# Kernel tuning notes

Measured on AMD Instinct MI355X. Metric: run time of the kernel, lower is better.

Reference implementation:

```python
import jax, jax.numpy as jnp
import numpy as np

N = 50000      # num nodes
E = 800000     # num edges (before self loops)
H = 2          # heads
C = 64         # out_channels (== in_dim, extra_layer=False)
L = 3          # n_layer
SLOPE = 0.2    # leaky_relu negative_slope


def setup_inputs() -> dict:
    key = jax.random.key(0)
    k1, k2, k3 = jax.random.split(key, 3)
    x = jax.random.normal(k1, (N, C), dtype=jnp.float32)
    edge_index = jax.random.randint(k2, (2, E), 0, N)
    att = jax.random.normal(k3, (L, H, C), dtype=jnp.float32) * 0.1  # glorot-ish scale
    bias = jnp.zeros((L, C), dtype=jnp.float32)
    return {"x": x, "edge_index": edge_index, "att": att, "bias": bias}


def _segment_softmax(alpha, dst, n):
    # alpha: [Etot, H], softmax over edges sharing the same destination node
    m = jax.ops.segment_max(alpha, dst, num_segments=n)          # [N, H]
    a = jnp.exp(alpha - m[dst])                                  # [Etot, H]
    s = jax.ops.segment_sum(a, dst, num_segments=n)              # [N, H]
    return a / (s[dst] + 1e-16)


def _gat_layer(x, src, dst, att_l, bias_l):
    # extra_layer=False: x_l == x_r == x broadcast over heads, so x_i + x_j is
    # head-independent; compute it once as [Etot, C].
    m = jax.nn.leaky_relu(x[dst] + x[src], negative_slope=SLOPE)  # [Etot, C]
    alpha = m @ att_l.T                                           # [Etot, H]
    alpha = _segment_softmax(alpha, dst, N)
    # message = x_j * alpha, scatter-add to destinations, then mean over heads
    outs = [jax.ops.segment_sum(x[src] * alpha[:, h:h + 1], dst, num_segments=N)
            for h in range(H)]                                    # H x [N, C]
    return jnp.stack(outs, 0).mean(0) + bias_l                    # [N, C]


def reference(x, edge_index, att, bias):
    # add self loops (add_self_loops=True)
    loops = jnp.arange(N, dtype=edge_index.dtype)
    src = jnp.concatenate([edge_index[0], loops])
    dst = jnp.concatenate([edge_index[1], loops])
    feats = [x]
    h = x
    for l in range(L):
        h = _gat_layer(h, src, dst, att[l], bias[l])
        feats.append(h)
    return jnp.stack(feats, axis=1).mean(axis=1)  # [N, C]
```

## Files before the change

### kernel.cpp

```cpp
#include <hip/hip_runtime.h>
#include <hip/hip_bf16.h>

#define NN 50000
#define EE 800000
#define CC 64
#define HH 2
#define LL 3
#define CAP 64
#define NB 782
#define BCAP 1280
#define CHUNK 8192
#define NBLK ((EE + CHUNK - 1) / CHUNK)



__global__ __launch_bounds__(1024) void k_bin(const int* __restrict__ ei,
                                              int* __restrict__ bcnt,
                                              unsigned int* __restrict__ bucket) {
    __shared__ unsigned int stash[CHUNK];
    __shared__ int hist[NB];
    __shared__ int rank[NB];
    __shared__ int base[NB];

    int c0 = blockIdx.x * CHUNK;
    int n = EE - c0; if (n > CHUNK) n = CHUNK;

    for (int b = threadIdx.x; b < NB; b += 1024) { hist[b] = 0; rank[b] = 0; }
    __syncthreads();

    for (int k = threadIdx.x; k < n; k += 1024) {
        unsigned int s = (unsigned int)ei[c0 + k];
        unsigned int d = (unsigned int)ei[EE + c0 + k];
        stash[k] = (d << 16) | s;
        atomicAdd(&hist[d >> 6], 1);
    }
    __syncthreads();

    for (int b = threadIdx.x; b < NB; b += 1024) {
        int c = hist[b];
        base[b] = c ? atomicAdd(&bcnt[b], c) : 0;
    }
    __syncthreads();

    for (int k = threadIdx.x; k < n; k += 1024) {
        unsigned int pk = stash[k];
        int b = (int)(pk >> 22);
        int r = atomicAdd(&rank[b], 1);
        int pos = base[b] + r;
        if (pos < BCAP) bucket[(size_t)b * BCAP + pos] = pk;
    }
}

__global__ __launch_bounds__(256) void k_place(const unsigned int* __restrict__ bucket,
                                               const int* __restrict__ bcnt,
                                               int* __restrict__ cnt,
                                               unsigned short* __restrict__ slots) {
    __shared__ int lcnt[64];
    int b = blockIdx.x;
    if (threadIdx.x < 64) lcnt[threadIdx.x] = 0;
    __syncthreads();
    int node0 = b << 6;
    int m = bcnt[b];
    if (m > BCAP) m = BCAP;
    const unsigned int* src = bucket + (size_t)b * BCAP;
    for (int i = threadIdx.x; i < m; i += 256) {
        unsigned int pk = src[i];
        int d = (int)(pk >> 16);
        int s = (int)(pk & 0xFFFFu);
        int pos = atomicAdd(&lcnt[d - node0], 1);
        if (pos < CAP) slots[(size_t)d * CAP + pos] = (unsigned short)s;
    }
    __syncthreads();
    if (threadIdx.x < 64) {
        int node = node0 + threadIdx.x;
        if (node < NN) cnt[node] = lcnt[threadIdx.x];
    }
}


typedef float v2f __attribute__((ext_vector_type(2)));

template <int CTRL>
__device__ __forceinline__ float dpp_add(float v) {
    int t = __builtin_amdgcn_update_dpp(0, __float_as_int(v), CTRL, 0xF, 0xF, true);
    return v + __int_as_float(t);
}

__device__ __forceinline__ float red16(float v) {
    v = dpp_add<0xB1>(v);
    v = dpp_add<0x4E>(v);
    v = dpp_add<0x141>(v);
    v = dpp_add<0x140>(v);
    return v;
}

__device__ __forceinline__ v2f lk2(v2f v) {
    v2f t = 0.2f * v;
    return __builtin_elementwise_max(v, t);
}

__device__ __forceinline__ v2f fma2(v2f a, v2f b, v2f c) {
    return __builtin_elementwise_fma(a, b, c);
}

template <bool FIRST>
__global__ __launch_bounds__(256) void k_gat(const float* __restrict__ h,
                                             const int* __restrict__ cnt,
                                             const unsigned short* __restrict__ slots,
                                             const float* __restrict__ att_l,
                                             const float* __restrict__ bias_l,
                                             float* __restrict__ h_out,
                                             float* __restrict__ acc, int n) {
    int wid = threadIdx.x >> 6;
    int lane = threadIdx.x & 63;
    int node = blockIdx.x * 4 + wid;
    if (node >= n) return;
    int sub = lane >> 4, q = lane & 15;
    unsigned qb = (unsigned)q << 4;
    const char* hb = (const char*)h;
    const v2f* attv = (const v2f*)att_l;
    v2f a0_01 = attv[2 * q],      a0_23 = attv[2 * q + 1];
    v2f a1_01 = attv[32 + 2 * q], a1_23 = attv[32 + 2 * q + 1];
    float4 hd = *(const float4*)(hb + (((unsigned)node << 8) + qb));
    v2f hd01 = {hd.x, hd.y}, hd23 = {hd.z, hd.w};
    int deg = cnt[node];
    if (deg > CAP) deg = CAP;
    const unsigned* rowu = (const unsigned*)(slots + (size_t)node * CAP);

    float s0, s1;
    v2f A0_01, A0_23, A1_01, A1_23;

    {
        v2f u01 = lk2(hd01 + hd01), u23 = lk2(hd23 + hd23);
        v2f d0 = fma2(u23, a0_23, u01 * a0_01);
        v2f d1 = fma2(u23, a1_23, u01 * a1_01);
        float p0 = red16(d0.x + d0.y);
        float p1 = red16(d1.x + d1.y);
        float e0 = 0.25f * __expf(p0), e1 = 0.25f * __expf(p1);
        s0 = e0; s1 = e1;
        A0_01 = e0 * hd01; A0_23 = e0 * hd23;
        A1_01 = e1 * hd01; A1_23 = e1 * hd23;
    }

    int npair = deg >> 1;
#pragma unroll 2
    for (int p = sub; p < npair; p += 4) {
        unsigned pk = rowu[p];
        float4 va = *(const float4*)(hb + (((pk & 0xFFFFu) << 8) + qb));
        float4 vb = *(const float4*)(hb + (((pk >> 16) << 8) + qb));
        v2f va01 = {va.x, va.y}, va23 = {va.z, va.w};
        v2f vb01 = {vb.x, vb.y}, vb23 = {vb.z, vb.w};
        v2f ma01 = lk2(va01 + hd01), ma23 = lk2(va23 + hd23);
        v2f mb01 = lk2(vb01 + hd01), mb23 = lk2(vb23 + hd23);
        v2f da0 = fma2(ma23, a0_23, ma01 * a0_01);
        v2f da1 = fma2(ma23, a1_23, ma01 * a1_01);
        v2f db0 = fma2(mb23, a0_23, mb01 * a0_01);
        v2f db1 = fma2(mb23, a1_23, mb01 * a1_01);
        float pa0 = red16(da0.x + da0.y);
        float pa1 = red16(da1.x + da1.y);
        float pb0 = red16(db0.x + db0.y);
        float pb1 = red16(db1.x + db1.y);
        float ea0 = __expf(pa0), ea1 = __expf(pa1);
        float eb0 = __expf(pb0), eb1 = __expf(pb1);
        s0 += ea0 + eb0;
        s1 += ea1 + eb1;
        v2f ea0v = {ea0, ea0}, ea1v = {ea1, ea1};
        v2f eb0v = {eb0, eb0}, eb1v = {eb1, eb1};
        A0_01 = fma2(ea0v, va01, fma2(eb0v, vb01, A0_01));
        A0_23 = fma2(ea0v, va23, fma2(eb0v, vb23, A0_23));
        A1_01 = fma2(ea1v, va01, fma2(eb1v, vb01, A1_01));
        A1_23 = fma2(ea1v, va23, fma2(eb1v, vb23, A1_23));
    }

    if (deg & 1) {
        int t = deg - 1;
        if (sub == ((t >> 1) & 3)) {
            unsigned s = ((const unsigned short*)rowu)[t];
            float4 hv = *(const float4*)(hb + ((s << 8) + qb));
            v2f hv01 = {hv.x, hv.y}, hv23 = {hv.z, hv.w};
            v2f m01 = lk2(hv01 + hd01), m23 = lk2(hv23 + hd23);
            v2f d0 = fma2(m23, a0_23, m01 * a0_01);
            v2f d1 = fma2(m23, a1_23, m01 * a1_01);
            float p0 = red16(d0.x + d0.y);
            float p1 = red16(d1.x + d1.y);
            float e0 = __expf(p0), e1 = __expf(p1);
            s0 += e0; s1 += e1;
            v2f e0v = {e0, e0}, e1v = {e1, e1};
            A0_01 = fma2(e0v, hv01, A0_01); A0_23 = fma2(e0v, hv23, A0_23);
            A1_01 = fma2(e1v, hv01, A1_01); A1_23 = fma2(e1v, hv23, A1_23);
        }
    }

#pragma unroll
    for (int step = 16; step <= 32; step <<= 1) {
        s0 += __shfl_xor(s0, step);
        s1 += __shfl_xor(s1, step);
        A0_01.x += __shfl_xor(A0_01.x, step); A0_01.y += __shfl_xor(A0_01.y, step);
        A0_23.x += __shfl_xor(A0_23.x, step); A0_23.y += __shfl_xor(A0_23.y, step);
        A1_01.x += __shfl_xor(A1_01.x, step); A1_01.y += __shfl_xor(A1_01.y, step);
        A1_23.x += __shfl_xor(A1_23.x, step); A1_23.y += __shfl_xor(A1_23.y, step);
    }

    if (sub == 0) {
        float inv0 = 0.5f / (s0 + 1e-16f);
        float inv1 = 0.5f / (s1 + 1e-16f);
        float4 b4 = ((const float4*)bias_l)[q];
        float4 o;
        o.x = A0_01.x * inv0 + A1_01.x * inv1 + b4.x;
        o.y = A0_01.y * inv0 + A1_01.y * inv1 + b4.y;
        o.z = A0_23.x * inv0 + A1_23.x * inv1 + b4.z;
        o.w = A0_23.y * inv0 + A1_23.y * inv1 + b4.w;
        ((float4*)h_out)[(size_t)node * 16 + q] = o;
        float4* accp = (float4*)acc + (size_t)node * 16 + q;
        float4 ac;
        if (FIRST) {
            ac.x = 0.25f * (hd.x + o.x); ac.y = 0.25f * (hd.y + o.y);
            ac.z = 0.25f * (hd.z + o.z); ac.w = 0.25f * (hd.w + o.w);
        } else {
            ac = *accp;
            ac.x += 0.25f * o.x; ac.y += 0.25f * o.y;
            ac.z += 0.25f * o.z; ac.w += 0.25f * o.w;
        }
        *accp = ac;
    }
}


static inline size_t align256(size_t x) { return (x + 255) & ~(size_t)255; }

extern "C" void kernel_launch(void* const* d_in, const int* in_sizes, int n_in,
                              void* d_out, int out_size, void* d_ws, size_t ws_size,
                              hipStream_t stream) {
    const float* x    = (const float*)d_in[0];
    const int*   ei   = (const int*)d_in[1];
    const float* att  = (const float*)d_in[2];
    const float* bias = (const float*)d_in[3];
    float* acc = (float*)d_out;

    char* w = (char*)d_ws;
    int* bcnt   = (int*)w;              w += align256((size_t)NB * sizeof(int));
    int* cnt    = (int*)w;              w += align256((size_t)NN * sizeof(int));
    unsigned int* bucket = (unsigned int*)w;
    w += align256((size_t)NB * BCAP * sizeof(unsigned int));
    unsigned short* slots = (unsigned short*)w;
    w += align256((size_t)NN * CAP * sizeof(unsigned short));
    float* hA   = (float*)w;            w += align256((size_t)NN * CC * sizeof(float));
    float* hB   = (float*)w;            w += align256((size_t)NN * CC * sizeof(float));

    const int B = 256;

    hipMemsetAsync(bcnt, 0, (size_t)NB * sizeof(int), stream);
    k_bin<<<NBLK, 1024, 0, stream>>>(ei, bcnt, bucket);
    k_place<<<NB, B, 0, stream>>>(bucket, bcnt, cnt, slots);

    k_gat<true><<<(NN + 3) / 4, B, 0, stream>>>(
        x, cnt, slots, att, bias, hA, acc, NN);
    k_gat<false><<<(NN + 3) / 4, B, 0, stream>>>(
        hA, cnt, slots, att + (size_t)HH * CC, bias + CC, hB, acc, NN);
    k_gat<false><<<(NN + 3) / 4, B, 0, stream>>>(
        hB, cnt, slots, att + (size_t)2 * HH * CC, bias + 2 * CC, hA, acc, NN);
}
```

Before: 196.1 us.

## Store node features in fp16 to halve gather traffic in GAT layers

Converts the input features to fp16 in a new kernel and keeps all intermediate layer outputs in fp16, so each gathered neighbor row is 128 bytes instead of 256. The lane mapping changes from 16 lanes x 4 floats to 8 lanes x 8 halves, giving 8 edge-pairs in flight per wave, with a new cross-group reduction. The last layer no longer writes its unused hidden output. This reduces memory bandwidth on the random gathers but adds fp16 rounding error that compounds across layers, plus an extra conversion launch.

```diff
diff --git a/kernel.cpp b/kernel.cpp
--- a/kernel.cpp
+++ b/kernel.cpp
@@ -1,5 +1,5 @@
 #include <hip/hip_runtime.h>
-#include <hip/hip_bf16.h>
+#include <hip/hip_fp16.h>
 
 #define NN 50000
 #define EE 800000
@@ -77,6 +77,17 @@
     }
 }
 
+__global__ __launch_bounds__(256) void k_cvt(const float* __restrict__ x,
+                                             unsigned short* __restrict__ x16) {
+    int i = blockIdx.x * 256 + threadIdx.x;
+    if (i >= NN * CC / 4) return;
+    float4 v = ((const float4*)x)[i];
+    __half2 h0 = __float22half2_rn((float2){v.x, v.y});
+    __half2 h1 = __float22half2_rn((float2){v.z, v.w});
+    uint2 u = {__builtin_bit_cast(unsigned, h0), __builtin_bit_cast(unsigned, h1)};
+    ((uint2*)x16)[i] = u;
+}
+
 
 typedef float v2f __attribute__((ext_vector_type(2)));
 
@@ -86,11 +97,17 @@
     return v + __int_as_float(t);
 }
 
-__device__ __forceinline__ float red16(float v) {
+__device__ __forceinline__ float red8(float v) {
     v = dpp_add<0xB1>(v);
     v = dpp_add<0x4E>(v);
     v = dpp_add<0x141>(v);
-    v = dpp_add<0x140>(v);
+    return v;
+}
+
+__device__ __forceinline__ float merge8(float v) {
+    v = dpp_add<0x128>(v);
+    v += __shfl_xor(v, 16);
+    v += __shfl_xor(v, 32);
     return v;
 }
 
@@ -103,125 +120,175 @@
     return __builtin_elementwise_fma(a, b, c);
 }
 
-template <bool FIRST>
-__global__ __launch_bounds__(256) void k_gat(const float* __restrict__ h,
+__device__ __forceinline__ void ldrow(const char* hbq, unsigned idx, v2f v[4]) {
+    uint4 u = *(const uint4*)(hbq + ((size_t)idx << 7));
+    float2 f0 = __half22float2(__builtin_bit_cast(__half2, u.x));
+    float2 f1 = __half22float2(__builtin_bit_cast(__half2, u.y));
+    float2 f2 = __half22float2(__builtin_bit_cast(__half2, u.z));
+    float2 f3 = __half22float2(__builtin_bit_cast(__half2, u.w));
+    v[0] = (v2f){f0.x, f0.y}; v[1] = (v2f){f1.x, f1.y};
+    v[2] = (v2f){f2.x, f2.y}; v[3] = (v2f){f3.x, f3.y};
+}
+
+template <bool FIRST, bool WRITE>
+__global__ __launch_bounds__(256) void k_gat(const unsigned short* __restrict__ hin,
+                                             const float* __restrict__ xf,
                                              const int* __restrict__ cnt,
                                              const unsigned short* __restrict__ slots,
                                              const float* __restrict__ att_l,
                                              const float* __restrict__ bias_l,
-                                             float* __restrict__ h_out,
+                                             unsigned short* __restrict__ hout,
                                              float* __restrict__ acc, int n) {
     int wid = threadIdx.x >> 6;
     int lane = threadIdx.x & 63;
     int node = blockIdx.x * 4 + wid;
     if (node >= n) return;
-    int sub = lane >> 4, q = lane & 15;
-    unsigned qb = (unsigned)q << 4;
-    const char* hb = (const char*)h;
+    int sub = lane >> 3;
+    unsigned t = (unsigned)(lane & 7);
+    const char* hbq = (const char*)hin + (t << 4);
     const v2f* attv = (const v2f*)att_l;
-    v2f a0_01 = attv[2 * q],      a0_23 = attv[2 * q + 1];
-    v2f a1_01 = attv[32 + 2 * q], a1_23 = attv[32 + 2 * q + 1];
-    float4 hd = *(const float4*)(hb + (((unsigned)node << 8) + qb));
-    v2f hd01 = {hd.x, hd.y}, hd23 = {hd.z, hd.w};
+    v2f a0[4], a1[4];
+#pragma unroll
+    for (int k = 0; k < 4; ++k) {
+        a0[k] = attv[4 * t + k];
+        a1[k] = attv[32 + 4 * t + k];
+    }
+    v2f hd[4];
+    ldrow(hbq, (unsigned)node, hd);
     int deg = cnt[node];
     if (deg > CAP) deg = CAP;
     const unsigned* rowu = (const unsigned*)(slots + (size_t)node * CAP);
 
     float s0, s1;
-    v2f A0_01, A0_23, A1_01, A1_23;
+    v2f A0[4], A1[4];
 
     {
-        v2f u01 = lk2(hd01 + hd01), u23 = lk2(hd23 + hd23);
-        v2f d0 = fma2(u23, a0_23, u01 * a0_01);
-        v2f d1 = fma2(u23, a1_23, u01 * a1_01);
-        float p0 = red16(d0.x + d0.y);
-        float p1 = red16(d1.x + d1.y);
-        float e0 = 0.25f * __expf(p0), e1 = 0.25f * __expf(p1);
+        v2f u[4];
+#pragma unroll
+        for (int k = 0; k < 4; ++k) u[k] = lk2(hd[k] + hd[k]);
+        v2f d0 = u[0] * a0[0], d1 = u[0] * a1[0];
+#pragma unroll
+        for (int k = 1; k < 4; ++k) {
+            d0 = fma2(u[k], a0[k], d0);
+            d1 = fma2(u[k], a1[k], d1);
+        }
+        float p0 = red8(d0.x + d0.y);
+        float p1 = red8(d1.x + d1.y);
+        float e0 = 0.125f * __expf(p0), e1 = 0.125f * __expf(p1);
         s0 = e0; s1 = e1;
-        A0_01 = e0 * hd01; A0_23 = e0 * hd23;
-        A1_01 = e1 * hd01; A1_23 = e1 * hd23;
+#pragma unroll
+        for (int k = 0; k < 4; ++k) { A0[k] = e0 * hd[k]; A1[k] = e1 * hd[k]; }
     }
 
     int npair = deg >> 1;
-#pragma unroll 2
-    for (int p = sub; p < npair; p += 4) {
+#pragma unroll 1
+    for (int p = sub; p < npair; p += 8) {
         unsigned pk = rowu[p];
-        float4 va = *(const float4*)(hb + (((pk & 0xFFFFu) << 8) + qb));
-        float4 vb = *(const float4*)(hb + (((pk >> 16) << 8) + qb));
-        v2f va01 = {va.x, va.y}, va23 = {va.z, va.w};
-        v2f vb01 = {vb.x, vb.y}, vb23 = {vb.z, vb.w};
-        v2f ma01 = lk2(va01 + hd01), ma23 = lk2(va23 + hd23);
-        v2f mb01 = lk2(vb01 + hd01), mb23 = lk2(vb23 + hd23);
-        v2f da0 = fma2(ma23, a0_23, ma01 * a0_01);
-        v2f da1 = fma2(ma23, a1_23, ma01 * a1_01);
-        v2f db0 = fma2(mb23, a0_23, mb01 * a0_01);
-        v2f db1 = fma2(mb23, a1_23, mb01 * a1_01);
-        float pa0 = red16(da0.x + da0.y);
-        float pa1 = red16(da1.x + da1.y);
-        float pb0 = red16(db0.x + db0.y);
-        float pb1 = red16(db1.x + db1.y);
+        v2f va[4], vb[4];
+        ldrow(hbq, pk & 0xFFFFu, va);
+        ldrow(hbq, pk >> 16, vb);
+        v2f ma[4], mb[4];
+#pragma unroll
+        for (int k = 0; k < 4; ++k) {
+            ma[k] = lk2(va[k] + hd[k]);
+            mb[k] = lk2(vb[k] + hd[k]);
+        }
+        v2f da0 = ma[0] * a0[0], da1 = ma[0] * a1[0];
+        v2f db0 = mb[0] * a0[0], db1 = mb[0] * a1[0];
+#pragma unroll
+        for (int k = 1; k < 4; ++k) {
+            da0 = fma2(ma[k], a0[k], da0); da1 = fma2(ma[k], a1[k], da1);
+            db0 = fma2(mb[k], a0[k], db0); db1 = fma2(mb[k], a1[k], db1);
+        }
+        float pa0 = red8(da0.x + da0.y);
+        float pa1 = red8(da1.x + da1.y);
+        float pb0 = red8(db0.x + db0.y);
+        float pb1 = red8(db1.x + db1.y);
         float ea0 = __expf(pa0), ea1 = __expf(pa1);
         float eb0 = __expf(pb0), eb1 = __expf(pb1);
         s0 += ea0 + eb0;
         s1 += ea1 + eb1;
         v2f ea0v = {ea0, ea0}, ea1v = {ea1, ea1};
         v2f eb0v = {eb0, eb0}, eb1v = {eb1, eb1};
-        A0_01 = fma2(ea0v, va01, fma2(eb0v, vb01, A0_01));
-        A0_23 = fma2(ea0v, va23, fma2(eb0v, vb23, A0_23));
-        A1_01 = fma2(ea1v, va01, fma2(eb1v, vb01, A1_01));
-        A1_23 = fma2(ea1v, va23, fma2(eb1v, vb23, A1_23));
+#pragma unroll
+        for (int k = 0; k < 4; ++k) {
+            A0[k] = fma2(ea0v, va[k], fma2(eb0v, vb[k], A0[k]));
+            A1[k] = fma2(ea1v, va[k], fma2(eb1v, vb[k], A1[k]));
+        }
     }
 
     if (deg & 1) {
-        int t = deg - 1;
-        if (sub == ((t >> 1) & 3)) {
-            unsigned s = ((const unsigned short*)rowu)[t];
-            float4 hv = *(const float4*)(hb + ((s << 8) + qb));
-            v2f hv01 = {hv.x, hv.y}, hv23 = {hv.z, hv.w};
-            v2f m01 = lk2(hv01 + hd01), m23 = lk2(hv23 + hd23);
-            v2f d0 = fma2(m23, a0_23, m01 * a0_01);
-            v2f d1 = fma2(m23, a1_23, m01 * a1_01);
-            float p0 = red16(d0.x + d0.y);
-            float p1 = red16(d1.x + d1.y);
+        int te = deg - 1;
+        if (sub == ((te >> 1) & 7)) {
+            unsigned s = ((const unsigned short*)rowu)[te];
+            v2f hv[4];
+            ldrow(hbq, s, hv);
+            v2f m[4];
+#pragma unroll
+            for (int k = 0; k < 4; ++k) m[k] = lk2(hv[k] + hd[k]);
+            v2f d0 = m[0] * a0[0], d1 = m[0] * a1[0];
+#pragma unroll
+            for (int k = 1; k < 4; ++k) {
+                d0 = fma2(m[k], a0[k], d0);
+                d1 = fma2(m[k], a1[k], d1);
+            }
+            float p0 = red8(d0.x + d0.y);
+            float p1 = red8(d1.x + d1.y);
             float e0 = __expf(p0), e1 = __expf(p1);
             s0 += e0; s1 += e1;
             v2f e0v = {e0, e0}, e1v = {e1, e1};
-            A0_01 = fma2(e0v, hv01, A0_01); A0_23 = fma2(e0v, hv23, A0_23);
-            A1_01 = fma2(e1v, hv01, A1_01); A1_23 = fma2(e1v, hv23, A1_23);
-        }
-    }
-
-#pragma unroll
-    for (int step = 16; step <= 32; step <<= 1) {
-        s0 += __shfl_xor(s0, step);
-        s1 += __shfl_xor(s1, step);
-        A0_01.x += __shfl_xor(A0_01.x, step); A0_01.y += __shfl_xor(A0_01.y, step);
-        A0_23.x += __shfl_xor(A0_23.x, step); A0_23.y += __shfl_xor(A0_23.y, step);
-        A1_01.x += __shfl_xor(A1_01.x, step); A1_01.y += __shfl_xor(A1_01.y, step);
-        A1_23.x += __shfl_xor(A1_23.x, step); A1_23.y += __shfl_xor(A1_23.y, step);
+#pragma unroll
+            for (int k = 0; k < 4; ++k) {
+                A0[k] = fma2(e0v, hv[k], A0[k]);
+                A1[k] = fma2(e1v, hv[k], A1[k]);
+            }
+        }
+    }
+
+    s0 = merge8(s0);
+    s1 = merge8(s1);
+    float inv0 = 0.5f / (s0 + 1e-16f);
+    float inv1 = 0.5f / (s1 + 1e-16f);
+    v2f o[4];
+#pragma unroll
+    for (int k = 0; k < 4; ++k) {
+        o[k] = inv0 * A0[k] + inv1 * A1[k];
+        o[k].x = merge8(o[k].x);
+        o[k].y = merge8(o[k].y);
     }
 
     if (sub == 0) {
-        float inv0 = 0.5f / (s0 + 1e-16f);
-        float inv1 = 0.5f / (s1 + 1e-16f);
-        float4 b4 = ((const float4*)bias_l)[q];
-        float4 o;
-        o.x = A0_01.x * inv0 + A1_01.x * inv1 + b4.x;
-        o.y = A0_01.y * inv0 + A1_01.y * inv1 + b4.y;
-        o.z = A0_23.x * inv0 + A1_23.x * inv1 + b4.z;
-        o.w = A0_23.y * inv0 + A1_23.y * inv1 + b4.w;
-        ((float4*)h_out)[(size_t)node * 16 + q] = o;
-        float4* accp = (float4*)acc + (size_t)node * 16 + q;
-        float4 ac;
+        const v2f* bv = (const v2f*)bias_l;
+#pragma unroll
+        for (int k = 0; k < 4; ++k) o[k] += bv[4 * t + k];
+        if constexpr (WRITE) {
+            __half2 w0 = __float22half2_rn((float2){o[0].x, o[0].y});
+            __half2 w1 = __float22half2_rn((float2){o[1].x, o[1].y});
+            __half2 w2 = __float22half2_rn((float2){o[2].x, o[2].y});
+            __half2 w3 = __float22half2_rn((float2){o[3].x, o[3].y});
+            uint4 u = {__builtin_bit_cast(unsigned, w0),
+                       __builtin_bit_cast(unsigned, w1),
+                       __builtin_bit_cast(unsigned, w2),
+                       __builtin_bit_cast(unsigned, w3)};
+            ((uint4*)hout)[(size_t)node * 8 + t] = u;
+        }
+        float4* accp = (float4*)acc + (size_t)node * 16 + 2 * t;
+        float4 c0, c1;
         if (FIRST) {
-            ac.x = 0.25f * (hd.x + o.x); ac.y = 0.25f * (hd.y + o.y);
-            ac.z = 0.25f * (hd.z + o.z); ac.w = 0.25f * (hd.w + o.w);
+            const float4* xr = (const float4*)xf + (size_t)node * 16 + 2 * t;
+            float4 x0 = xr[0], x1 = xr[1];
+            c0.x = 0.25f * (x0.x + o[0].x); c0.y = 0.25f * (x0.y + o[0].y);
+            c0.z = 0.25f * (x0.z + o[1].x); c0.w = 0.25f * (x0.w + o[1].y);
+            c1.x = 0.25f * (x1.x + o[2].x); c1.y = 0.25f * (x1.y + o[2].y);
+            c1.z = 0.25f * (x1.z + o[3].x); c1.w = 0.25f * (x1.w + o[3].y);
         } else {
-            ac = *accp;
-            ac.x += 0.25f * o.x; ac.y += 0.25f * o.y;
-            ac.z += 0.25f * o.z; ac.w += 0.25f * o.w;
-        }
-        *accp = ac;
+            c0 = accp[0]; c1 = accp[1];
+            c0.x += 0.25f * o[0].x; c0.y += 0.25f * o[0].y;
+            c0.z += 0.25f * o[1].x; c0.w += 0.25f * o[1].y;
+            c1.x += 0.25f * o[2].x; c1.y += 0.25f * o[2].y;
+            c1.z += 0.25f * o[3].x; c1.w += 0.25f * o[3].y;
+        }
+        accp[0] = c0; accp[1] = c1;
     }
 }
 
@@ -243,20 +310,27 @@
     unsigned int* bucket = (unsigned int*)w;
     w += align256((size_t)NB * BCAP * sizeof(unsigned int));
     unsigned short* slots = (unsigned short*)w;
-    w += align256((size_t)NN * CAP * sizeof(unsigned short));
-    float* hA   = (float*)w;            w += align256((size_t)NN * CC * sizeof(float));
-    float* hB   = (float*)w;            w += align256((size_t)NN * CC * sizeof(float));
+    w += align256((size_t)NN * CAP * sizeof(unsigned short) + 256);
+    unsigned short* x16 = (unsigned short*)w;
+    w += align256((size_t)NN * CC * sizeof(__half));
+    unsigned short* hA16 = (unsigned short*)w;
+    w += align256((size_t)NN * CC * sizeof(__half));
+    unsigned short* hB16 = (unsigned short*)w;
+    w += align256((size_t)NN * CC * sizeof(__half));
 
     const int B = 256;
-
+    const int GG = (NN + 3) / 4;
+
+    k_cvt<<<(NN * CC / 4 + B - 1) / B, B, 0, stream>>>(x, x16);
     hipMemsetAsync(bcnt, 0, (size_t)NB * sizeof(int), stream);
     k_bin<<<NBLK, 1024, 0, stream>>>(ei, bcnt, bucket);
     k_place<<<NB, B, 0, stream>>>(bucket, bcnt, cnt, slots);
 
-    k_gat<true><<<(NN + 3) / 4, B, 0, stream>>>(
-        x, cnt, slots, att, bias, hA, acc, NN);
-    k_gat<false><<<(NN + 3) / 4, B, 0, stream>>>(
-        hA, cnt, slots, att + (size_t)HH * CC, bias + CC, hB, acc, NN);
-    k_gat<false><<<(NN + 3) / 4, B, 0, stream>>>(
-        hB, cnt, slots, att + (size_t)2 * HH * CC, bias + 2 * CC, hA, acc, NN);
-}
+    k_gat<true, true><<<GG, B, 0, stream>>>(
+        x16, x, cnt, slots, att, bias, hA16, acc, NN);
+    k_gat<false, true><<<GG, B, 0, stream>>>(
+        hA16, nullptr, cnt, slots, att + (size_t)HH * CC, bias + CC, hB16, acc, NN);
+    k_gat<false, false><<<GG, B, 0, stream>>>(
+        hB16, nullptr, cnt, slots, att + (size_t)2 * HH * CC, bias + 2 * CC,
+        nullptr, acc, NN);
+}
```

Result: slower. 232.7 us (+18.7%).
